# Kernel optimization log

Hardware: AMD Instinct MI355X
Metric: run time of the kernel (lower is better)

## Reference

```python
import jax, jax.numpy as jnp
import numpy as np

B, R, K, C, H, E = 256, 6, 49, 512, 1024, 300
NV, NR, NL = 504, 190, 2001


def setup_inputs() -> dict:
    key = jax.random.key(0)
    ks = list(jax.random.split(key, 40))
    it = iter(ks)

    def nrm(shape, s=0.02):
        return jax.random.normal(next(it), shape, jnp.float32) * s

    return dict(
        v_org=jax.random.normal(next(it), (B, C, 7, 7), jnp.float32),
        img_feat=jax.random.normal(next(it), (B, K, C), jnp.float32),
        gt_verb=jax.random.randint(next(it), (B,), 0, NV),
        role_idx=jax.random.randint(next(it), (B, R), 0, NR),
        mask=jnp.ones((B, R, R), jnp.int32),
        verb_table=nrm((NV, E)),
        role_table=nrm((NR, E)),
        qc_W=nrm((2 * E, H)), qc_b=jnp.zeros((H,), jnp.float32),
        av_W=nrm((C, H)), av_b=jnp.zeros((H,), jnp.float32),
        aq_W=nrm((H, H)), aq_b=jnp.zeros((H,), jnp.float32),
        ao_W=nrm((H, 1)), ao_b=jnp.zeros((1,), jnp.float32),
        vn_W=nrm((C, H)), vn_b=jnp.zeros((H,), jnp.float32),
        qn_W=nrm((H, H)), qn_b=jnp.zeros((H,), jnp.float32),
        Wq=nrm((H, H)), Wk=nrm((H, H)), Wv=nrm((H, H)), Wo=nrm((H, H)),
        uqc_W=nrm((H + 2 * E, H)), uqc_b=jnp.zeros((H,), jnp.float32),
        cls_W=nrm((H, NL)), cls_b=jnp.zeros((NL,), jnp.float32),
    )


def _mfb(q_repr, v_repr):
    # elementwise MFB pool (n_heads=1 -> sumpool is identity), sign-sqrt, L2 norm
    z = q_repr * v_repr
    s = jnp.sqrt(jax.nn.relu(z)) - jnp.sqrt(jax.nn.relu(-z))
    n = jnp.sqrt(jnp.sum(s * s, axis=1, keepdims=True))
    return s / jnp.maximum(n, 1e-12)


def _v_att(img, q_emb, av_W, av_b, aq_W, aq_b, ao_W, ao_b):
    v = jax.nn.relu(img @ av_W + av_b)            # [N,K,H]
    q = jax.nn.relu(q_emb @ aq_W + aq_b)          # [N,H]
    logits = (v * q[:, None, :]) @ ao_W + ao_b    # [N,K,1]
    return jax.nn.softmax(logits, axis=1)


def reference(v_org, img_feat, gt_verb, role_idx, mask, verb_table, role_table,
              qc_W, qc_b, av_W, av_b, aq_W, aq_b, ao_W, ao_b,
              vn_W, vn_b, qn_W, qn_b, Wq, Wk, Wv, Wo,
              uqc_W, uqc_b, cls_W, cls_b):
    Bn, Cn, h, w = v_org.shape
    Rn = role_idx.shape[1]
    img0 = v_org.reshape(Bn, Cn, h * w).transpose(0, 2, 1)          # [B,K,C]
    img = jnp.broadcast_to(img0[:, None], (Bn, Rn, h * w, Cn)).reshape(Bn * Rn, h * w, Cn)
    Kv, Cv = img_feat.shape[1], img_feat.shape[2]
    img_v = jnp.broadcast_to(img_feat[:, None], (Bn, Rn, Kv, Cv)).reshape(Bn * Rn, Kv, Cv)

    verb_e = verb_table[gt_verb]                                     # [B,E]
    role_e = role_table[role_idx]                                    # [B,R,E]
    rv = jnp.concatenate([jnp.broadcast_to(verb_e[:, None], (Bn, Rn, verb_e.shape[-1])), role_e], -1)
    rv = rv.reshape(Bn * Rn, -1)                                     # [BR,2E]

    q_emb = jax.nn.relu(rv @ qc_W + qc_b)

    att = _v_att(img, q_emb, av_W, av_b, aq_W, aq_b, ao_W, ao_b)
    v_emb = (att * img).sum(1)
    v_repr = jax.nn.relu(v_emb @ vn_W + vn_b)
    q_repr = jax.nn.relu(q_emb @ qn_W + qn_b)
    out = _mfb(q_repr, v_repr)
    ans0 = out

    att_v = _v_att(img_v, q_emb, av_W, av_b, aq_W, aq_b, ao_W, ao_b)
    v_repr_verb = jax.nn.relu((att_v * img_v).sum(1) @ vn_W + vn_b)
    out_verb = _mfb(q_repr, v_repr_verb)

    # masked neighbour attention over role nodes (single head)
    Hd = out.shape[-1]
    cur = out.reshape(Bn, Rn, Hd)
    qh, kh, vh = cur @ Wq, cur @ Wk, cur @ Wv
    scores = jnp.einsum('bid,bjd->bij', qh, kh) / jnp.sqrt(jnp.float32(Hd))
    m = mask.astype(jnp.float32) * (1.0 - jnp.eye(Rn, dtype=jnp.float32))  # no self edges
    scores = jnp.where(m > 0, scores, jnp.float32(-1e9))
    attn = jax.nn.softmax(scores, axis=-1)
    neigh = (jnp.einsum('bij,bjd->bid', attn, vh) @ Wo).reshape(Bn * Rn, Hd)

    uq = jax.nn.relu(jnp.concatenate([neigh, rv], -1) @ uqc_W + uqc_b)
    att2 = _v_att(img, uq, av_W, av_b, aq_W, aq_b, ao_W, ao_b)
    v_repr2 = jax.nn.relu((att2 * img).sum(1) @ vn_W + vn_b)
    q_repr2 = jax.nn.relu(uq @ qn_W + qn_b)
    out2 = _mfb(q_repr2, v_repr2)

    gate = jax.nn.sigmoid(out2 + out_verb)
    out_f = (1.0 - gate) * out_verb + gate * jnp.tanh(out2 + ans0)

    logits = out_f @ cls_W + cls_b
    return logits.reshape(Bn, Rn, -1)
```

## Files before the change

kernel.cpp:

```cpp
#include <hip/hip_runtime.h>
#include <math.h>

typedef unsigned short u16;
typedef __attribute__((ext_vector_type(8))) short short8;
typedef __attribute__((ext_vector_type(4))) float f32x4;

#define Bb 256
#define Rr 6
#define Ksp 49
#define Cc 512
#define Hh 1024
#define Ee 300
#define NN (Bb*Rr)
#define NLl 2001

__device__ __forceinline__ u16 f2b(float x) {
    union { float f; unsigned u; } c; c.f = x;
    unsigned r = c.u + 0x7fffu + ((c.u >> 16) & 1u);
    return (u16)(r >> 16);
}
__device__ __forceinline__ float b2f(u16 b) {
    union { unsigned u; float f; } c; c.u = ((unsigned)b) << 16; return c.f;
}

#define ASYNC16(gp, lp) __builtin_amdgcn_global_load_lds( \
    (const __attribute__((address_space(1))) unsigned int*)(gp), \
    (__attribute__((address_space(3))) unsigned int*)(lp), 16, 0, 0)

constexpr size_t O_QC   = 0;
constexpr size_t O_AV   = O_QC   + (size_t)1024*640;
constexpr size_t O_AQQN = O_AV   + (size_t)1024*512;
constexpr size_t O_VN   = O_AQQN + (size_t)2048*1024;
constexpr size_t O_QKV  = O_VN   + (size_t)1024*512;
constexpr size_t O_WO   = O_QKV  + (size_t)3072*1024;
constexpr size_t O_UQC  = O_WO   + (size_t)1024*1024;
constexpr size_t O_CLS  = O_UQC  + (size_t)1024*1664;
constexpr size_t WT_ELEMS = O_CLS + (size_t)2048*1024;

template<int TAG, int BM, int BN, int BK>
__global__ void __launch_bounds__(256) gemm_bf16(
    const u16* __restrict__ A, int lda, const u16* __restrict__ Bt,
    const float* __restrict__ bias,
    u16* __restrict__ Cb, int ldcb, float* __restrict__ Cf, int ldcf,
    int K, int split, int Nreal, int act)
{
    constexpr int SM = BM / 16, SN = BN / 16;
    constexpr int KG = BK / 32;
    constexpr int WM = BM / 32, WN = BN / 32;
    constexpr int BUF = (SM + SN) * KG * 512;
    __shared__ u16 lds[2 * BUF];
    const int tid  = threadIdx.x;
    const int wave = tid >> 6, lane = tid & 63;
    const int m0 = lane & 15, q0 = lane >> 4;

    const int gn = gridDim.x;
    const int nblk = gn * gridDim.y;
    const int lid = blockIdx.y * gn + blockIdx.x;
    const int per = nblk >> 3, rem = nblk & 7;
    const int xcd = lid & 7, slot = lid >> 3;
    const int t = xcd * per + ((xcd < rem) ? xcd : rem) + slot;
    const int tm = t / gn, tn = t - tm * gn;
    const int bm = tm * BM, bn = tn * BN;
    const int wr = wave >> 1, wc = wave & 1;

    auto stage = [&](int kt, int buf) {
        u16* l = &lds[buf * BUF];
        #pragma unroll
        for (int s = wave; s < SM; s += 4)
            #pragma unroll
            for (int g = 0; g < KG; g++) {
                const u16* gp = A + (size_t)(bm + s * 16 + m0) * lda + kt + g * 32 + q0 * 8;
                ASYNC16(gp, &l[(s * KG + g) * 512]);
            }
        #pragma unroll
        for (int s = wave; s < SN; s += 4)
            #pragma unroll
            for (int g = 0; g < KG; g++) {
                const u16* gp = Bt + (size_t)(bn + s * 16 + m0) * K + kt + g * 32 + q0 * 8;
                ASYNC16(gp, &l[(SM * KG + s * KG + g) * 512]);
            }
    };

    f32x4 acc[WM][WN];
    #pragma unroll
    for (int i = 0; i < WM; i++)
        #pragma unroll
        for (int j = 0; j < WN; j++)
            acc[i][j] = (f32x4){0.f, 0.f, 0.f, 0.f};

    stage(0, 0);
    const int nIter = K / BK;
    for (int it = 0; it < nIter; ++it) {
        __syncthreads();
        if (it + 1 < nIter) stage((it + 1) * BK, (it + 1) & 1);
        const u16* l = &lds[(it & 1) * BUF];
        short8 af[WM][KG], bf[WN][KG];
        #pragma unroll
        for (int i = 0; i < WM; i++)
            #pragma unroll
            for (int g = 0; g < KG; g++)
                af[i][g] = *(const short8*)&l[(((wr * WM + i) * KG + g) * 64 + lane) * 8];
        #pragma unroll
        for (int j = 0; j < WN; j++)
            #pragma unroll
            for (int g = 0; g < KG; g++)
                bf[j][g] = *(const short8*)&l[((SM * KG + (wc * WN + j) * KG + g) * 64 + lane) * 8];
        #pragma unroll
        for (int g = 0; g < KG; g++)
            #pragma unroll
            for (int i = 0; i < WM; i++)
                #pragma unroll
                for (int j = 0; j < WN; j++)
                    acc[i][j] = __builtin_amdgcn_mfma_f32_16x16x32_bf16(
                        af[i][g], bf[j][g], acc[i][j], 0, 0, 0);
    }

    #pragma unroll
    for (int i = 0; i < WM; i++) {
        #pragma unroll
        for (int j = 0; j < WN; j++) {
            const int col = bn + (wc * WN + j) * 16 + m0;
            if (col >= Nreal) continue;
            const float bv = bias ? bias[col] : 0.f;
            #pragma unroll
            for (int r = 0; r < 4; r++) {
                const int row = bm + (wr * WM + i) * 16 + q0 * 4 + r;
                float v = acc[i][j][r] + bv;
                if (act) v = fmaxf(v, 0.f);
                if (col < split) Cb[(size_t)row * ldcb + col] = f2b(v);
                else             Cf[(size_t)row * ldcf + col - split] = v;
            }
        }
    }
}

struct PrepSrc { const float* s[11]; };

__global__ void __launch_bounds__(256) prep_kernel(
    PrepSrc ps, u16* __restrict__ wt,
    const float* __restrict__ verb_table, const float* __restrict__ role_table,
    const int* __restrict__ gt_verb, const int* __restrict__ role_idx,
    u16* __restrict__ cat,
    const float* __restrict__ v_org, u16* __restrict__ A1,
    const float* __restrict__ img_feat, u16* __restrict__ A2,
    const float* __restrict__ aq_b, const float* __restrict__ qn_b,
    float* __restrict__ aqqn_b)
{
    __shared__ float sm[64 * 50];
    const int bid = blockIdx.x, tid = threadIdx.x;

    if (bid < 11520) {
        const int tStart[12] = {0,640,1152,2176,3200,3712,4736,5760,6784,7808,9472,11520};
        const int tK[11]  = {600,512,1024,1024,512,1024,1024,1024,1024,1624,1024};
        const int tN[11]  = {1024,1024,1024,1024,1024,1024,1024,1024,1024,1024,2001};
        const int tKp[11] = {640,512,1024,1024,512,1024,1024,1024,1024,1664,1024};
        const int tNp[11] = {1024,1024,1024,1024,1024,1024,1024,1024,1024,1024,2048};
        const long tDst[11] = {(long)O_QC,(long)O_AV,(long)O_AQQN,(long)(O_AQQN+1048576),
                               (long)O_VN,(long)O_QKV,(long)(O_QKV+1048576),
                               (long)(O_QKV+2097152),(long)O_WO,(long)O_UQC,(long)O_CLS};
        int e = 0;
        while (bid >= tStart[e + 1]) e++;
        const int local = bid - tStart[e];
        const int ktiles = tKp[e] >> 5;
        const int bx = local % ktiles, by = local / ktiles;
        const float* W = ps.s[e];
        u16* Wt = wt + tDst[e];
        const int K = tK[e], Nn = tN[e], Kp = tKp[e], Np = tNp[e];
        const int kt = bx * 32, nt = by * 32;
        const int tx = tid & 31, ty = tid >> 5;
        for (int i = ty; i < 32; i += 8) {
            const int k = kt + i, n = nt + tx;
            sm[i * 33 + tx] = (k < K && n < Nn) ? W[(size_t)k * Nn + n] : 0.f;
        }
        __syncthreads();
        for (int i = ty; i < 32; i += 8) {
            const int n = nt + i, k = kt + tx;
            if (n < Np && k < Kp) Wt[(size_t)n * Kp + k] = f2b(sm[tx * 33 + i]);
        }
    } else if (bid < 15360) {
        const int idx = (bid - 11520) * 256 + tid;
        const int n = idx / 640;
        const int col = idx - n * 640;
        const int b = n / Rr, r = n - b * Rr;
        float v = 0.f;
        if (col < Ee)          v = verb_table[(size_t)gt_verb[b] * Ee + col];
        else if (col < 2 * Ee) v = role_table[(size_t)role_idx[b * Rr + r] * Ee + (col - Ee)];
        cat[(size_t)n * 1664 + 1024 + col] = f2b(v);
    } else if (bid < 17408) {
        const int local = bid - 15360;
        const int b = local >> 3, c0 = (local & 7) << 6;
        {
            const int ci = tid >> 2, k0 = tid & 3;
            const float* p = v_org + ((size_t)b * Cc + c0 + ci) * Ksp;
            for (int k = k0; k < Ksp; k += 4) sm[ci * 50 + k] = p[k];
        }
        __syncthreads();
        {
            const int cc = tid & 63, kb = tid >> 6;
            for (int k = kb; k < Ksp; k += 4)
                A1[((size_t)b * Ksp + k) * Cc + c0 + cc] = f2b(sm[cc * 50 + k]);
        }
    } else if (bid < 23680) {
        const int i = (bid - 17408) * 256 + tid;
        const float4 v = ((const float4*)img_feat)[i];
        ushort4 o;
        o.x = f2b(v.x); o.y = f2b(v.y); o.z = f2b(v.z); o.w = f2b(v.w);
        ((ushort4*)A2)[i] = o;
    } else {
        const int i = (bid - 23680) * 256 + tid;
        if (i < 2048) aqqn_b[i] = (i < 1024) ? aq_b[i] : qn_b[i - 1024];
    }
}

__global__ void __launch_bounds__(256) att_kernel(
    const u16* __restrict__ Vh0,
    const u16* __restrict__ Q,
    const float* __restrict__ aoW, const float* __restrict__ aoB,
    const u16* __restrict__ IMG0,
    u16* __restrict__ Vemb0)
{
    const int task = blockIdx.x >> 8;
    const int b = blockIdx.x & 255;
    const u16* Vh   = Vh0   + (size_t)task * 12544 * 1024;
    const u16* IMGb = IMG0  + (size_t)task * 12544 * 512;
    u16* Vemb       = Vemb0 + (size_t)task * NN * 512;
    const int tid = threadIdx.x, wave = tid >> 6, lane = tid & 63;
    __shared__ u16 s_qs[16][1032];
    __shared__ float s_log[64][6];
    __shared__ float s_att[49][6];

    for (int n = 0; n < 16; n++) {
        const u16* qp = Q + ((size_t)b * Rr + n) * Hh;
        for (int h = tid; h < 1032; h += 256) {
            u16 v = 0;
            if (n < Rr && h < Hh) v = f2b(b2f(qp[h]) * aoW[h]);
            s_qs[n][h] = v;
        }
    }
    __syncthreads();

    const int m = lane & 15, q = lane >> 4;
    {
        f32x4 acc = (f32x4){0.f, 0.f, 0.f, 0.f};
        const u16* arow = Vh + ((size_t)b * Ksp + wave * 16 + m) * Hh + q * 8;
        const u16* brow = &s_qs[m][q * 8];
        for (int kt = 0; kt < Hh; kt += 32) {
            const short8 af = *(const short8*)(arow + kt);
            const short8 bf = *(const short8*)(brow + kt);
            acc = __builtin_amdgcn_mfma_f32_16x16x32_bf16(af, bf, acc, 0, 0, 0);
        }
        const float aob = aoB[0];
        #pragma unroll
        for (int r = 0; r < 4; r++) {
            const int k = wave * 16 + q * 4 + r;
            if (k < Ksp && m < Rr) s_log[k][m] = acc[r] + aob;
        }
    }
    __syncthreads();

    if (wave == 0) {
        for (int r = 0; r < Rr; r++) {
            const float v = (lane < Ksp) ? s_log[lane][r] : -INFINITY;
            float mx = v;
            #pragma unroll
            for (int off = 32; off; off >>= 1) mx = fmaxf(mx, __shfl_down(mx, off));
            mx = __shfl(mx, 0);
            const float e = (lane < Ksp) ? expf(v - mx) : 0.f;
            float s = e;
            #pragma unroll
            for (int off = 32; off; off >>= 1) s += __shfl_down(s, off);
            s = __shfl(s, 0);
            if (lane < Ksp) s_att[lane][r] = e / s;
        }
    }
    __syncthreads();

    float acc2[Rr][2];
    #pragma unroll
    for (int r = 0; r < Rr; r++) { acc2[r][0] = 0.f; acc2[r][1] = 0.f; }
    const u16* ib = IMGb + (size_t)b * Ksp * Cc + tid * 2;
    #pragma unroll 7
    for (int k = 0; k < Ksp; k++) {
        const ushort2 v = *(const ushort2*)(ib + (size_t)k * Cc);
        const float v0 = b2f(v.x), v1 = b2f(v.y);
        #pragma unroll
        for (int r = 0; r < Rr; r++) {
            const float w = s_att[k][r];
            acc2[r][0] += w * v0; acc2[r][1] += w * v1;
        }
    }
    #pragma unroll
    for (int r = 0; r < Rr; r++) {
        ushort2 o; o.x = f2b(acc2[r][0]); o.y = f2b(acc2[r][1]);
        *(ushort2*)(Vemb + ((size_t)b * Rr + r) * Cc + tid * 2) = o;
    }
}

__global__ void __launch_bounds__(256) mfb2_kernel(
    const float* __restrict__ q, const float* __restrict__ v,
    float* __restrict__ a0f, u16* __restrict__ a0b, float* __restrict__ vbf)
{
    const int n = blockIdx.x;
    const int qrow = (n < NN) ? n : n - NN;
    const int tid = threadIdx.x;
    __shared__ float red[4];
    float sv[4];
    float local = 0.f;
    #pragma unroll
    for (int i = 0; i < 4; i++) {
        const int h = tid + i * 256;
        const float z = q[(size_t)qrow * Hh + h] * v[(size_t)n * Hh + h];
        const float s = (z > 0.f) ? sqrtf(z) : -sqrtf(-z);
        sv[i] = s;
        local += s * s;
    }
    #pragma unroll
    for (int off = 32; off; off >>= 1) local += __shfl_down(local, off);
    if ((tid & 63) == 0) red[tid >> 6] = local;
    __syncthreads();
    const float tot = red[0] + red[1] + red[2] + red[3];
    const float inv = 1.f / fmaxf(sqrtf(tot), 1e-12f);
    #pragma unroll
    for (int i = 0; i < 4; i++) {
        const float o = sv[i] * inv;
        if (n < NN) {
            const size_t off2 = (size_t)n * Hh + tid + i * 256;
            a0f[off2] = o; a0b[off2] = f2b(o);
        } else {
            vbf[(size_t)(n - NN) * Hh + tid + i * 256] = o;
        }
    }
}

__global__ void __launch_bounds__(256) mfb_gate_kernel(
    const float* __restrict__ q, const float* __restrict__ v,
    const float* __restrict__ ovb, const float* __restrict__ oa0,
    u16* __restrict__ outb)
{
    const int n = blockIdx.x;
    const int tid = threadIdx.x;
    __shared__ float red[4];
    float sv[4];
    float local = 0.f;
    #pragma unroll
    for (int i = 0; i < 4; i++) {
        const int h = tid + i * 256;
        const float z = q[(size_t)n * Hh + h] * v[(size_t)n * Hh + h];
        const float s = (z > 0.f) ? sqrtf(z) : -sqrtf(-z);
        sv[i] = s;
        local += s * s;
    }
    #pragma unroll
    for (int off = 32; off; off >>= 1) local += __shfl_down(local, off);
    if ((tid & 63) == 0) red[tid >> 6] = local;
    __syncthreads();
    const float tot = red[0] + red[1] + red[2] + red[3];
    const float inv = 1.f / fmaxf(sqrtf(tot), 1e-12f);
    #pragma unroll
    for (int i = 0; i < 4; i++) {
        const size_t off2 = (size_t)n * Hh + tid + i * 256;
        const float o2 = sv[i] * inv;
        const float ov = ovb[off2], a0 = oa0[off2];
        const float g = 1.f / (1.f + expf(-(o2 + ov)));
        outb[off2] = f2b((1.f - g) * ov + g * tanhf(o2 + a0));
    }
}

__global__ void __launch_bounds__(256) nattn_kernel(
    const u16* __restrict__ qkv, const int* __restrict__ mask,
    u16* __restrict__ nv)
{
    const int b = blockIdx.x;
    const int tid = threadIdx.x;
    __shared__ float s_sc[Rr][Rr];
    __shared__ float s_at[Rr][Rr];
    const int wave = tid >> 6, lane = tid & 63;
    for (int p = wave; p < Rr * Rr; p += 4) {
        const int i = p / Rr, j = p - (p / Rr) * Rr;
        const u16* qp = qkv + ((size_t)(b * Rr + i)) * 3072;
        const u16* kp = qkv + ((size_t)(b * Rr + j)) * 3072 + 1024;
        float s = 0.f;
        for (int h = lane * 2; h < Hh; h += 128) {
            const ushort2 qv = *(const ushort2*)(qp + h);
            const ushort2 kv = *(const ushort2*)(kp + h);
            s += b2f(qv.x) * b2f(kv.x) + b2f(qv.y) * b2f(kv.y);
        }
        #pragma unroll
        for (int off = 32; off; off >>= 1) s += __shfl_down(s, off);
        if (lane == 0) s_sc[i][j] = s * 0.03125f;
    }
    __syncthreads();
    if (tid < Rr) {
        const int i = tid;
        float vals[Rr];
        float m = -INFINITY;
        #pragma unroll
        for (int j = 0; j < Rr; j++) {
            const float mij = (i == j) ? 0.f : (float)mask[b * Rr * Rr + i * Rr + j];
            const float v = (mij > 0.f) ? s_sc[i][j] : -1e9f;
            vals[j] = v;
            m = fmaxf(m, v);
        }
        float ssum = 0.f;
        #pragma unroll
        for (int j = 0; j < Rr; j++) { const float e = expf(vals[j] - m); s_at[i][j] = e; ssum += e; }
        const float invs = 1.f / ssum;
        #pragma unroll
        for (int j = 0; j < Rr; j++) s_at[i][j] *= invs;
    }
    __syncthreads();
    for (int h = tid; h < Hh; h += 256) {
        #pragma unroll
        for (int i = 0; i < Rr; i++) {
            float acc = 0.f;
            #pragma unroll
            for (int j = 0; j < Rr; j++)
                acc += s_at[i][j] * b2f(qkv[((size_t)(b * Rr + j)) * 3072 + 2048 + h]);
            nv[((size_t)(b * Rr + i)) * Hh + h] = f2b(acc);
        }
    }
}

extern "C" void kernel_launch(void* const* d_in, const int* in_sizes, int n_in,
                              void* d_out, int out_size, void* d_ws, size_t ws_size,
                              hipStream_t stream)
{
    const float* v_org      = (const float*)d_in[0];
    const float* img_feat   = (const float*)d_in[1];
    const int*   gt_verb    = (const int*)d_in[2];
    const int*   role_idx   = (const int*)d_in[3];
    const int*   mask       = (const int*)d_in[4];
    const float* verb_table = (const float*)d_in[5];
    const float* role_table = (const float*)d_in[6];
    const float* qc_W  = (const float*)d_in[7];
    const float* qc_b  = (const float*)d_in[8];
    const float* av_W  = (const float*)d_in[9];
    const float* av_b  = (const float*)d_in[10];
    const float* aq_W  = (const float*)d_in[11];
    const float* aq_b  = (const float*)d_in[12];
    const float* ao_W  = (const float*)d_in[13];
    const float* ao_b  = (const float*)d_in[14];
    const float* vn_W  = (const float*)d_in[15];
    const float* vn_b  = (const float*)d_in[16];
    const float* qn_W  = (const float*)d_in[17];
    const float* qn_b  = (const float*)d_in[18];
    const float* Wq    = (const float*)d_in[19];
    const float* Wk    = (const float*)d_in[20];
    const float* Wv    = (const float*)d_in[21];
    const float* Wo    = (const float*)d_in[22];
    const float* uqc_W = (const float*)d_in[23];
    const float* uqc_b = (const float*)d_in[24];
    const float* cls_W = (const float*)d_in[25];
    const float* cls_b = (const float*)d_in[26];
    float* out = (float*)d_out;

    char* base = (char*)d_ws;
    size_t off = 0;
    auto alloc = [&](size_t bytes) -> char* {
        char* p = base + off;
        off += (bytes + 255) & ~(size_t)255;
        return p;
    };
    u16* wt = (u16*)alloc(WT_ELEMS * 2);
    u16* A1 = (u16*)alloc((size_t)12544 * 512 * 2 * 2);
    u16* A2 = A1 + (size_t)12544 * 512;
    u16* v_img = (u16*)alloc((size_t)12544 * 1024 * 2 * 2);
    u16* v_imgv = v_img + (size_t)12544 * 1024;
    u16* qkv = (u16*)v_imgv;
    u16* nv  = (u16*)((char*)v_imgv + (size_t)NN * 3072 * 2);
    u16* cat    = (u16*)alloc((size_t)NN * 1664 * 2);
    u16* q_emb  = (u16*)alloc((size_t)NN * 1024 * 2);
    u16* q_att  = (u16*)alloc((size_t)NN * 1024 * 2);
    u16* uq     = (u16*)alloc((size_t)NN * 1024 * 2);
    u16* out_f  = (u16*)alloc((size_t)NN * 1024 * 2);
    u16* v_emb2 = (u16*)alloc((size_t)2 * NN * 512 * 2);
    float* v_rep2 = (float*)alloc((size_t)2 * NN * 1024 * 4);
    float* q_rep = (float*)alloc((size_t)NN * 1024 * 4);
    float* a0f   = (float*)alloc((size_t)NN * 1024 * 4);
    u16*   a0b   = (u16*)alloc((size_t)NN * 1024 * 2);
    float* vbf   = (float*)alloc((size_t)NN * 1024 * 4);
    float* aqqn_b = (float*)alloc(2048 * 4);

    const dim3 blk(256);

    PrepSrc ps;
    ps.s[0] = qc_W;  ps.s[1] = av_W; ps.s[2] = aq_W; ps.s[3] = qn_W;
    ps.s[4] = vn_W;  ps.s[5] = Wq;   ps.s[6] = Wk;   ps.s[7] = Wv;
    ps.s[8] = Wo;    ps.s[9] = uqc_W; ps.s[10] = cls_W;
    prep_kernel<<<dim3(23688), blk, 0, stream>>>(
        ps, wt, verb_table, role_table, gt_verb, role_idx, cat,
        v_org, A1, img_feat, A2, aq_b, qn_b, aqqn_b);

    gemm_bf16<2,32,64,128><<<dim3(16, 48), blk, 0, stream>>>(
        cat + 1024, 1664, wt + O_QC, qc_b, q_emb, 1024, nullptr, 0,
        640, 1024, 1024, 1);
    gemm_bf16<3,128,128,32><<<dim3(8, 196), blk, 0, stream>>>(
        A1, 512, wt + O_AV, av_b, v_img, 1024, nullptr, 0,
        512, 1024, 1024, 1);
    gemm_bf16<4,32,64,128><<<dim3(32, 48), blk, 0, stream>>>(
        q_emb, 1024, wt + O_AQQN, aqqn_b, q_att, 1024, q_rep, 1024,
        1024, 1024, 2048, 1);
    att_kernel<<<dim3(512), blk, 0, stream>>>(v_img, q_att, ao_W, ao_b, A1, v_emb2);
    gemm_bf16<6,32,64,128><<<dim3(16, 96), blk, 0, stream>>>(
        v_emb2, 512, wt + O_VN, vn_b, nullptr, 0, v_rep2, 1024,
        512, 0, 1024, 1);
    mfb2_kernel<<<dim3(2 * NN), blk, 0, stream>>>(q_rep, v_rep2, a0f, a0b, vbf);
    gemm_bf16<8,32,64,128><<<dim3(48, 48), blk, 0, stream>>>(
        a0b, 1024, wt + O_QKV, nullptr, qkv, 3072, nullptr, 0,
        1024, 3072, 3072, 0);
    nattn_kernel<<<dim3(Bb), blk, 0, stream>>>(qkv, mask, nv);
    gemm_bf16<10,32,64,128><<<dim3(16, 48), blk, 0, stream>>>(
        nv, 1024, wt + O_WO, nullptr, cat, 1664, nullptr, 0,
        1024, 1024, 1024, 0);
    gemm_bf16<11,32,64,128><<<dim3(16, 48), blk, 0, stream>>>(
        cat, 1664, wt + O_UQC, uqc_b, uq, 1024, nullptr, 0,
        1664, 1024, 1024, 1);
    gemm_bf16<12,32,64,128><<<dim3(32, 48), blk, 0, stream>>>(
        uq, 1024, wt + O_AQQN, aqqn_b, q_att, 1024, q_rep, 1024,
        1024, 1024, 2048, 1);
    att_kernel<<<dim3(Bb), blk, 0, stream>>>(v_img, q_att, ao_W, ao_b, A1, v_emb2);
    gemm_bf16<14,32,64,128><<<dim3(16, 48), blk, 0, stream>>>(
        v_emb2, 512, wt + O_VN, vn_b, nullptr, 0, v_rep2, 1024,
        512, 0, 1024, 1);
    mfb_gate_kernel<<<dim3(NN), blk, 0, stream>>>(q_rep, v_rep2, vbf, a0f, out_f);
    gemm_bf16<16,32,64,128><<<dim3(32, 48), blk, 0, stream>>>(
        out_f, 1024, wt + O_CLS, cls_b, nullptr, 0, out, 2001,
        1024, 0, 2001, 0);
}
```

Baseline: 608.6 us.

## Fold Wv·Wo into one weight and precompute uqc role-part with qc GEMM

Precomputes (Wv@Wo) inside a combined GEMM kernel that also runs the av projection, so the separate Wo GEMM after neighbour attention disappears. nattn now writes straight into the concat buffer. The uqc matmul is split so its role/verb half is computed alongside the qc GEMM, and the remaining half adds that partial result in the epilogue. This removes two mid-pipeline GEMM launches and their K work, at the cost of an extra weight-product GEMM per call, a different bf16 rounding order, and an extra fp32 buffer.

```diff
diff --git a/kernel.cpp b/kernel.cpp
--- a/kernel.cpp
+++ b/kernel.cpp
@@ -28,19 +28,21 @@
     (__attribute__((address_space(3))) unsigned int*)(lp), 16, 0, 0)
 
 constexpr size_t O_QC   = 0;
-constexpr size_t O_AV   = O_QC   + (size_t)1024*640;
+constexpr size_t O_UQCB = O_QC   + (size_t)1024*640;
+constexpr size_t O_AV   = O_UQCB + (size_t)1024*640;
 constexpr size_t O_AQQN = O_AV   + (size_t)1024*512;
 constexpr size_t O_VN   = O_AQQN + (size_t)2048*1024;
 constexpr size_t O_QKV  = O_VN   + (size_t)1024*512;
 constexpr size_t O_WO   = O_QKV  + (size_t)3072*1024;
-constexpr size_t O_UQC  = O_WO   + (size_t)1024*1024;
-constexpr size_t O_CLS  = O_UQC  + (size_t)1024*1664;
-constexpr size_t WT_ELEMS = O_CLS + (size_t)2048*1024;
+constexpr size_t O_UQCT = O_WO   + (size_t)1024*1024;
+constexpr size_t O_CLS  = O_UQCT + (size_t)1024*1024;
+constexpr size_t O_WVP  = O_CLS  + (size_t)2048*1024;
+constexpr size_t WT_ELEMS = O_WVP + (size_t)2048*1024;
 
 template<int TAG, int BM, int BN, int BK>
 __global__ void __launch_bounds__(256) gemm_bf16(
     const u16* __restrict__ A, int lda, const u16* __restrict__ Bt,
-    const float* __restrict__ bias,
+    const float* __restrict__ bias, const float* __restrict__ Cadd, int ldadd,
     u16* __restrict__ Cb, int ldcb, float* __restrict__ Cf, int ldcf,
     int K, int split, int Nreal, int act)
 {
@@ -126,11 +128,105 @@
             for (int r = 0; r < 4; r++) {
                 const int row = bm + (wr * WM + i) * 16 + q0 * 4 + r;
                 float v = acc[i][j][r] + bv;
-                if (act) v = fmaxf(v, 0.f);
-                if (col < split) Cb[(size_t)row * ldcb + col] = f2b(v);
-                else             Cf[(size_t)row * ldcf + col - split] = v;
+                if (Cadd) v += Cadd[(size_t)row * ldadd + col];
+                if (col < split) {
+                    if (act & 1) v = fmaxf(v, 0.f);
+                    Cb[(size_t)row * ldcb + col] = f2b(v);
+                } else {
+                    if (act & 2) v = fmaxf(v, 0.f);
+                    Cf[(size_t)row * ldcf + col - split] = v;
+                }
             }
         }
+    }
+}
+
+struct BT { const u16* A; int lda; const u16* Bt; const float* bias;
+            u16* C; int ldc; int K; int act; int gnx; };
+
+__global__ void __launch_bounds__(256) gemm_big2(BT t0, BT t1, int blocks0)
+{
+    __shared__ u16 lds[17408];
+    const int tid  = threadIdx.x;
+    const int wave = tid >> 6, lane = tid & 63;
+    const int m0 = lane & 15, q0 = lane >> 4;
+
+    const int nblk = gridDim.x;
+    const int lid = blockIdx.x;
+    const int per = nblk >> 3, rem = nblk & 7;
+    const int xcd = lid & 7, slot = lid >> 3;
+    const int t = xcd * per + ((xcd < rem) ? xcd : rem) + slot;
+    const BT T = (t < blocks0) ? t0 : t1;
+    const int tt = (t < blocks0) ? t : t - blocks0;
+    const int tm = tt / T.gnx, tn = tt - tm * T.gnx;
+    const int bm = tm * 128, bn = tn * 128;
+    const int wr = wave >> 1, wc = wave & 1;
+
+    auto stage = [&](int kt, int buf) {
+        u16* l = &lds[buf * 8192];
+        #pragma unroll
+        for (int s = wave; s < 8; s += 4) {
+            const u16* gp = T.A + (size_t)(bm + s * 16 + m0) * T.lda + kt + q0 * 8;
+            ASYNC16(gp, &l[s * 512]);
+        }
+        #pragma unroll
+        for (int s = wave; s < 8; s += 4) {
+            const u16* gp = T.Bt + (size_t)(bn + s * 16 + m0) * T.K + kt + q0 * 8;
+            ASYNC16(gp, &l[(8 + s) * 512]);
+        }
+    };
+
+    f32x4 acc[4][4];
+    #pragma unroll
+    for (int i = 0; i < 4; i++)
+        #pragma unroll
+        for (int j = 0; j < 4; j++)
+            acc[i][j] = (f32x4){0.f, 0.f, 0.f, 0.f};
+
+    stage(0, 0);
+    const int nIter = T.K >> 5;
+    for (int it = 0; it < nIter; ++it) {
+        __syncthreads();
+        if (it + 1 < nIter) stage((it + 1) * 32, (it + 1) & 1);
+        const u16* l = &lds[(it & 1) * 8192];
+        short8 af[4], bf[4];
+        #pragma unroll
+        for (int i = 0; i < 4; i++)
+            af[i] = *(const short8*)&l[((wr * 4 + i) * 64 + lane) * 8];
+        #pragma unroll
+        for (int j = 0; j < 4; j++)
+            bf[j] = *(const short8*)&l[((8 + wc * 4 + j) * 64 + lane) * 8];
+        #pragma unroll
+        for (int i = 0; i < 4; i++)
+            #pragma unroll
+            for (int j = 0; j < 4; j++)
+                acc[i][j] = __builtin_amdgcn_mfma_f32_16x16x32_bf16(
+                    af[i], bf[j], acc[i][j], 0, 0, 0);
+    }
+
+    __syncthreads();
+    #pragma unroll
+    for (int i = 0; i < 4; i++) {
+        #pragma unroll
+        for (int j = 0; j < 4; j++) {
+            const int cl = (wc * 4 + j) * 16 + m0;
+            const float bv = T.bias ? T.bias[bn + cl] : 0.f;
+            #pragma unroll
+            for (int r = 0; r < 4; r++) {
+                const int rl = (wr * 4 + i) * 16 + q0 * 4 + r;
+                float v = acc[i][j][r] + bv;
+                if (T.act) v = fmaxf(v, 0.f);
+                lds[rl * 136 + cl] = f2b(v);
+            }
+        }
+    }
+    __syncthreads();
+    #pragma unroll
+    for (int pass = 0; pass < 8; pass++) {
+        const int rl = pass * 16 + (tid >> 4);
+        const int c8 = (tid & 15) * 8;
+        const short8 v = *(const short8*)&lds[rl * 136 + c8];
+        *(short8*)(T.C + (size_t)(bm + rl) * T.ldc + bn + c8) = v;
     }
 }
 
@@ -143,21 +239,23 @@
     u16* __restrict__ cat,
     const float* __restrict__ v_org, u16* __restrict__ A1,
     const float* __restrict__ img_feat, u16* __restrict__ A2,
+    const float* __restrict__ Wv,
     const float* __restrict__ aq_b, const float* __restrict__ qn_b,
-    float* __restrict__ aqqn_b)
+    const float* __restrict__ qc_b,
+    float* __restrict__ aqqn_b, float* __restrict__ qcz_b)
 {
     __shared__ float sm[64 * 50];
     const int bid = blockIdx.x, tid = threadIdx.x;
 
-    if (bid < 11520) {
-        const int tStart[12] = {0,640,1152,2176,3200,3712,4736,5760,6784,7808,9472,11520};
-        const int tK[11]  = {600,512,1024,1024,512,1024,1024,1024,1024,1624,1024};
+    if (bid < 10496) {
+        const int tStart[12] = {0,640,1152,2176,3200,3712,4736,5760,6784,7808,8448,10496};
+        const int tK[11]  = {600,512,1024,1024,512,1024,1024,1024,1024,600,1024};
         const int tN[11]  = {1024,1024,1024,1024,1024,1024,1024,1024,1024,1024,2001};
-        const int tKp[11] = {640,512,1024,1024,512,1024,1024,1024,1024,1664,1024};
+        const int tKp[11] = {640,512,1024,1024,512,1024,1024,1024,1024,640,1024};
         const int tNp[11] = {1024,1024,1024,1024,1024,1024,1024,1024,1024,1024,2048};
         const long tDst[11] = {(long)O_QC,(long)O_AV,(long)O_AQQN,(long)(O_AQQN+1048576),
                                (long)O_VN,(long)O_QKV,(long)(O_QKV+1048576),
-                               (long)(O_QKV+2097152),(long)O_WO,(long)O_UQC,(long)O_CLS};
+                               (long)O_WO,(long)O_UQCT,(long)O_UQCB,(long)O_CLS};
         int e = 0;
         while (bid >= tStart[e + 1]) e++;
         const int local = bid - tStart[e];
@@ -177,8 +275,8 @@
             const int n = nt + i, k = kt + tx;
             if (n < Np && k < Kp) Wt[(size_t)n * Kp + k] = f2b(sm[tx * 33 + i]);
         }
-    } else if (bid < 15360) {
-        const int idx = (bid - 11520) * 256 + tid;
+    } else if (bid < 14336) {
+        const int idx = (bid - 10496) * 256 + tid;
         const int n = idx / 640;
         const int col = idx - n * 640;
         const int b = n / Rr, r = n - b * Rr;
@@ -186,8 +284,8 @@
         if (col < Ee)          v = verb_table[(size_t)gt_verb[b] * Ee + col];
         else if (col < 2 * Ee) v = role_table[(size_t)role_idx[b * Rr + r] * Ee + (col - Ee)];
         cat[(size_t)n * 1664 + 1024 + col] = f2b(v);
-    } else if (bid < 17408) {
-        const int local = bid - 15360;
+    } else if (bid < 16384) {
+        const int local = bid - 14336;
         const int b = local >> 3, c0 = (local & 7) << 6;
         {
             const int ci = tid >> 2, k0 = tid & 3;
@@ -200,24 +298,32 @@
             for (int k = kb; k < Ksp; k += 4)
                 A1[((size_t)b * Ksp + k) * Cc + c0 + cc] = f2b(sm[cc * 50 + k]);
         }
-    } else if (bid < 23680) {
-        const int i = (bid - 17408) * 256 + tid;
+    } else if (bid < 22656) {
+        const int i = (bid - 16384) * 256 + tid;
         const float4 v = ((const float4*)img_feat)[i];
         ushort4 o;
         o.x = f2b(v.x); o.y = f2b(v.y); o.z = f2b(v.z); o.w = f2b(v.w);
         ((ushort4*)A2)[i] = o;
+    } else if (bid < 23680) {
+        const int i = (bid - 22656) * 256 + tid;
+        const float4 v = ((const float4*)Wv)[i];
+        ushort4 o;
+        o.x = f2b(v.x); o.y = f2b(v.y); o.z = f2b(v.z); o.w = f2b(v.w);
+        ((ushort4*)(wt + O_WVP))[i] = o;
     } else {
         const int i = (bid - 23680) * 256 + tid;
-        if (i < 2048) aqqn_b[i] = (i < 1024) ? aq_b[i] : qn_b[i - 1024];
+        if (i < 2048)      aqqn_b[i] = (i < 1024) ? aq_b[i] : qn_b[i - 1024];
+        else if (i < 4096) {
+            const int k = i - 2048;
+            qcz_b[k] = (k < 1024) ? qc_b[k] : 0.f;
+        }
     }
 }
 
 __global__ void __launch_bounds__(256) att_kernel(
-    const u16* __restrict__ Vh0,
-    const u16* __restrict__ Q,
+    const u16* __restrict__ Vh0, const u16* __restrict__ Q,
     const float* __restrict__ aoW, const float* __restrict__ aoB,
-    const u16* __restrict__ IMG0,
-    u16* __restrict__ Vemb0)
+    const u16* __restrict__ IMG0, u16* __restrict__ Vemb0)
 {
     const int task = blockIdx.x >> 8;
     const int b = blockIdx.x & 255;
@@ -368,7 +474,7 @@
 
 __global__ void __launch_bounds__(256) nattn_kernel(
     const u16* __restrict__ qkv, const int* __restrict__ mask,
-    u16* __restrict__ nv)
+    u16* __restrict__ outp, int ldout)
 {
     const int b = blockIdx.x;
     const int tid = threadIdx.x;
@@ -416,7 +522,7 @@
             #pragma unroll
             for (int j = 0; j < Rr; j++)
                 acc += s_at[i][j] * b2f(qkv[((size_t)(b * Rr + j)) * 3072 + 2048 + h]);
-            nv[((size_t)(b * Rr + i)) * Hh + h] = f2b(acc);
+            outp[((size_t)(b * Rr + i)) * ldout + h] = f2b(acc);
         }
     }
 }
@@ -467,7 +573,6 @@
     u16* v_img = (u16*)alloc((size_t)12544 * 1024 * 2 * 2);
     u16* v_imgv = v_img + (size_t)12544 * 1024;
     u16* qkv = (u16*)v_imgv;
-    u16* nv  = (u16*)((char*)v_imgv + (size_t)NN * 3072 * 2);
     u16* cat    = (u16*)alloc((size_t)NN * 1664 * 2);
     u16* q_emb  = (u16*)alloc((size_t)NN * 1024 * 2);
     u16* q_att  = (u16*)alloc((size_t)NN * 1024 * 2);
@@ -479,51 +584,52 @@
     float* a0f   = (float*)alloc((size_t)NN * 1024 * 4);
     u16*   a0b   = (u16*)alloc((size_t)NN * 1024 * 2);
     float* vbf   = (float*)alloc((size_t)NN * 1024 * 4);
+    float* pre_uq = (float*)alloc((size_t)NN * 1024 * 4);
     float* aqqn_b = (float*)alloc(2048 * 4);
+    float* qcz_b  = (float*)alloc(2048 * 4);
 
     const dim3 blk(256);
 
     PrepSrc ps;
-    ps.s[0] = qc_W;  ps.s[1] = av_W; ps.s[2] = aq_W; ps.s[3] = qn_W;
-    ps.s[4] = vn_W;  ps.s[5] = Wq;   ps.s[6] = Wk;   ps.s[7] = Wv;
-    ps.s[8] = Wo;    ps.s[9] = uqc_W; ps.s[10] = cls_W;
-    prep_kernel<<<dim3(23688), blk, 0, stream>>>(
+    ps.s[0] = qc_W; ps.s[1] = av_W; ps.s[2] = aq_W; ps.s[3] = qn_W;
+    ps.s[4] = vn_W; ps.s[5] = Wq;   ps.s[6] = Wk;   ps.s[7] = Wo;
+    ps.s[8] = uqc_W; ps.s[9] = uqc_W + (size_t)1024 * 1024; ps.s[10] = cls_W;
+    prep_kernel<<<dim3(23696), blk, 0, stream>>>(
         ps, wt, verb_table, role_table, gt_verb, role_idx, cat,
-        v_org, A1, img_feat, A2, aq_b, qn_b, aqqn_b);
-
-    gemm_bf16<2,32,64,128><<<dim3(16, 48), blk, 0, stream>>>(
-        cat + 1024, 1664, wt + O_QC, qc_b, q_emb, 1024, nullptr, 0,
-        640, 1024, 1024, 1);
-    gemm_bf16<3,128,128,32><<<dim3(8, 196), blk, 0, stream>>>(
-        A1, 512, wt + O_AV, av_b, v_img, 1024, nullptr, 0,
-        512, 1024, 1024, 1);
+        v_org, A1, img_feat, A2, Wv, aq_b, qn_b, qc_b, aqqn_b, qcz_b);
+
+    BT t0 = { A1, 512, wt + O_AV, av_b, v_img, 1024, 512, 1, 8 };
+    BT t1 = { wt + O_WO, 1024, wt + O_WVP, nullptr,
+              wt + O_QKV + (size_t)2 * 1024 * 1024, 1024, 1024, 0, 8 };
+    gemm_big2<<<dim3(1568 + 64), blk, 0, stream>>>(t0, t1, 1568);
+
+    gemm_bf16<3,32,64,128><<<dim3(32, 48), blk, 0, stream>>>(
+        cat + 1024, 1664, wt + O_QC, qcz_b, nullptr, 0,
+        q_emb, 1024, pre_uq, 1024, 640, 1024, 2048, 1);
     gemm_bf16<4,32,64,128><<<dim3(32, 48), blk, 0, stream>>>(
-        q_emb, 1024, wt + O_AQQN, aqqn_b, q_att, 1024, q_rep, 1024,
-        1024, 1024, 2048, 1);
+        q_emb, 1024, wt + O_AQQN, aqqn_b, nullptr, 0,
+        q_att, 1024, q_rep, 1024, 1024, 1024, 2048, 3);
     att_kernel<<<dim3(512), blk, 0, stream>>>(v_img, q_att, ao_W, ao_b, A1, v_emb2);
     gemm_bf16<6,32,64,128><<<dim3(16, 96), blk, 0, stream>>>(
-        v_emb2, 512, wt + O_VN, vn_b, nullptr, 0, v_rep2, 1024,
-        512, 0, 1024, 1);
+        v_emb2, 512, wt + O_VN, vn_b, nullptr, 0,
+        nullptr, 0, v_rep2, 1024, 512, 0, 1024, 2);
     mfb2_kernel<<<dim3(2 * NN), blk, 0, stream>>>(q_rep, v_rep2, a0f, a0b, vbf);
     gemm_bf16<8,32,64,128><<<dim3(48, 48), blk, 0, stream>>>(
-        a0b, 1024, wt + O_QKV, nullptr, qkv, 3072, nullptr, 0,
-        1024, 3072, 3072, 0);
-    nattn_kernel<<<dim3(Bb), blk, 0, stream>>>(qkv, mask, nv);
+        a0b, 1024, wt + O_QKV, nullptr, nullptr, 0,
+        qkv, 3072, nullptr, 0, 1024, 3072, 3072, 0);
+    nattn_kernel<<<dim3(Bb), blk, 0, stream>>>(qkv, mask, cat, 1664);
     gemm_bf16<10,32,64,128><<<dim3(16, 48), blk, 0, stream>>>(
-        nv, 1024, wt + O_WO, nullptr, cat, 1664, nullptr, 0,
-        1024, 1024, 1024, 0);
-    gemm_bf16<11,32,64,128><<<dim3(16, 48), blk, 0, stream>>>(
-        cat, 1664, wt + O_UQC, uqc_b, uq, 1024, nullptr, 0,
-        1664, 1024, 1024, 1);
-    gemm_bf16<12,32,64,128><<<dim3(32, 48), blk, 0, stream>>>(
-        uq, 1024, wt + O_AQQN, aqqn_b, q_att, 1024, q_rep, 1024,
-        1024, 1024, 2048, 1);
+        cat, 1664, wt + O_UQCT, uqc_b, pre_uq, 1024,
+        uq, 1024, nullptr, 0, 1024, 1024, 1024, 1);
+    gemm_bf16<11,32,64,128><<<dim3(32, 48), blk, 0, stream>>>(
+        uq, 1024, wt + O_AQQN, aqqn_b, nullptr, 0,
+        q_att, 1024, q_rep, 1024, 1024, 1024, 2048, 3);
     att_kernel<<<dim3(Bb), blk, 0, stream>>>(v_img, q_att, ao_W, ao_b, A1, v_emb2);
-    gemm_bf16<14,32,64,128><<<dim3(16, 48), blk, 0, stream>>>(
-        v_emb2, 512, wt + O_VN, vn_b, nullptr, 0, v_rep2, 1024,
-        512, 0, 1024, 1);
+    gemm_bf16<13,32,64,128><<<dim3(16, 48), blk, 0, stream>>>(
+        v_emb2, 512, wt + O_VN, vn_b, nullptr, 0,
+        nullptr, 0, v_rep2, 1024, 512, 0, 1024, 2);
     mfb_gate_kernel<<<dim3(NN), blk, 0, stream>>>(q_rep, v_rep2, vbf, a0f, out_f);
-    gemm_bf16<16,32,64,128><<<dim3(32, 48), blk, 0, stream>>>(
-        out_f, 1024, wt + O_CLS, cls_b, nullptr, 0, out, 2001,
-        1024, 0, 2001, 0);
-}
+    gemm_bf16<15,32,64,128><<<dim3(32, 48), blk, 0, stream>>>(
+        out_f, 1024, wt + O_CLS, cls_b, nullptr, 0,
+        nullptr, 0, out, 2001, 1024, 0, 2001, 0);
+}
```

Measured after the change: 599.9 us. No clear change (-1.4%).
